# Optimization experiments

Measured on AMD Instinct MI355X. Metric: run time of the kernel, lower is better.

The kernel has to match this reference:

```python
import jax, jax.numpy as jnp
import numpy as np

N = 100000      # nodes
E = 1600000     # edges (avg degree 16)
IN = 128        # input_dim
H = 8           # heads
D = 8           # hidden_dim (== heads, required by the diversity-loss bmm)
HD = H * D      # per-layer width
OUT = 10        # output_dim
G = 64          # graphs in batch
NEG = 0.2       # GATConv leaky_relu slope
DIVW = 0.1      # diversity_weight


def setup_inputs() -> dict:
    key = jax.random.key(0)
    ks = jax.random.split(key, 20)
    w = lambda k, shape, fan: (jax.random.normal(k, shape, jnp.float32) / np.sqrt(fan)).astype(jnp.float32)
    inp = {}
    inp['x'] = jax.random.normal(ks[0], (N, IN), jnp.float32)
    inp['edge_index'] = jax.random.randint(ks[1], (2, E), 0, N, dtype=jnp.int32)
    inp['batch'] = jnp.sort(jax.random.randint(ks[2], (N,), 0, G, dtype=jnp.int32))
    # layer 0: GATConv(IN -> D, heads=H)
    inp['W0'] = w(ks[3], (IN, HD), IN)
    inp['att_src0'] = w(ks[4], (H, D), D)
    inp['att_dst0'] = w(ks[5], (H, D), D)
    inp['b0'] = jnp.zeros((HD,), jnp.float32)
    inp['gamma0'] = jnp.ones((HD,), jnp.float32)
    inp['beta0'] = jnp.zeros((HD,), jnp.float32)
    inp['P0'] = w(ks[6], (H, D), D)
    # layer 1: GATConv(HD -> D, heads=H)
    inp['W1'] = w(ks[7], (HD, HD), HD)
    inp['att_src1'] = w(ks[8], (H, D), D)
    inp['att_dst1'] = w(ks[9], (H, D), D)
    inp['b1'] = jnp.zeros((HD,), jnp.float32)
    inp['gamma1'] = jnp.ones((HD,), jnp.float32)
    inp['beta1'] = jnp.zeros((HD,), jnp.float32)
    inp['P1'] = w(ks[10], (H, D), D)
    inp['fc_W'] = w(ks[11], (HD, OUT), HD)
    inp['fc_b'] = jnp.zeros((OUT,), jnp.float32)
    return inp


def _gat(x, src, dst, W, a_src, a_dst, b):
    h = (x @ W).reshape(-1, H, D)                       # [N,H,D]
    al = jnp.sum(h * a_src, -1)                          # [N,H] src scores
    ar = jnp.sum(h * a_dst, -1)                          # [N,H] dst scores
    e = jax.nn.leaky_relu(al[src] + ar[dst], NEG)        # [E,H]
    m = jax.ops.segment_max(e, dst, num_segments=N)      # per-dst max (stable softmax)
    m = jnp.where(jnp.isfinite(m), m, 0.0)
    ex = jnp.exp(e - m[dst])
    den = jax.ops.segment_sum(ex, dst, num_segments=N)
    a = ex / (den[dst] + 1e-16)                          # PyG softmax eps
    out = jax.ops.segment_sum(a[:, :, None] * h[src], dst, num_segments=N)  # [N,H,D]
    return out.reshape(-1, HD) + b


def _bn(x, g, b):  # BatchNorm1d, training-mode batch stats, eps=1e-5
    mu = x.mean(0)
    var = x.var(0)
    return g * (x - mu) * jax.lax.rsqrt(var + 1e-5) + b


def _div_loss(x, P):
    xr = x.reshape(-1, H, D)
    pr = jnp.einsum('nij,jk->nik', xr, P)                # bmm with shared projector (needs D==H)
    nh = pr / jnp.maximum(jnp.linalg.norm(pr, axis=-1, keepdims=True), 1e-8)
    S = jnp.einsum('nid,njd->ij', nh, nh) / x.shape[0]   # mean-over-nodes cosine sims [H,H]
    iu = jnp.triu_indices(H, 1)
    return jnp.mean(S[iu] ** 2)


def reference(x, edge_index, batch, W0, att_src0, att_dst0, b0, gamma0, beta0, P0,
              W1, att_src1, att_dst1, b1, gamma1, beta1, P1, fc_W, fc_b):
    src, dst = edge_index[0], edge_index[1]
    dl = 0.0
    h = _gat(x, src, dst, W0, att_src0, att_dst0, b0)
    dl = dl + _div_loss(h, P0)
    h = jax.nn.elu(_bn(h, gamma0, beta0))
    h = _gat(h, src, dst, W1, att_src1, att_dst1, b1)
    dl = dl + _div_loss(h, P1)
    h = jax.nn.elu(_bn(h, gamma1, beta1))
    cnt = jax.ops.segment_sum(jnp.ones((N,), h.dtype), batch, num_segments=G)
    pooled = jax.ops.segment_sum(h, batch, num_segments=G) / jnp.maximum(cnt, 1.0)[:, None]
    logits = pooled @ fc_W + fc_b
    return logits, DIVW * dl
```

## Files before the change

### kernel.cpp

```cpp
#include <hip/hip_runtime.h>
#include <hip/hip_fp16.h>

#define NB 100000
#define NE 1600000
#define PSH 12500
#define BCAP 64
#define SCB 2048
#define GMB 1568
#define MIXB 3136

typedef int iv4 __attribute__((ext_vector_type(4)));

__device__ __forceinline__ float elu_f(float x) { return x > 0.f ? x : expm1f(x); }

__global__ __launch_bounds__(256) void k_fill_zero(float4* __restrict__ p, int n4) {
    int i = blockIdx.x * 256 + threadIdx.x, s = gridDim.x * 256;
    float4 z = make_float4(0.f, 0.f, 0.f, 0.f);
    for (; i < n4; i += s) p[i] = z;
}

__global__ __launch_bounds__(256) void k_scat_gemm(
    const iv4* __restrict__ src4, const iv4* __restrict__ dst4,
    int* __restrict__ cnt, int* __restrict__ buck, int ne4,
    const float* __restrict__ X, const float* __restrict__ W,
    const float* __restrict__ attS, const float* __restrict__ attD,
    __half* __restrict__ Hout, float* __restrict__ al, float* __restrict__ ar, int nrows)
{
    __shared__ float4 xs4[64][8];
    __shared__ float  ws_[32][64];
    int b = blockIdx.x, t = threadIdx.x;
    int isS, idx;
    if (b < MIXB) {
        int g = b >> 3;
        isS = g & 1;
        idx = (g >> 1) * 8 + (b & 7);
    } else {
        isS = 1;
        idx = GMB + (b - MIXB);
    }

    if (isS) {
        int part = idx & 7;
        unsigned lo = part * PSH;
        int pb = idx >> 3;
        int st = (SCB >> 3) * 256;
        int i  = pb * 256 + t;
        int i2 = i + st;
        int st2 = st * 2;
        for (; i2 < ne4; i += st2, i2 += st2) {
            iv4 dA = dst4[i];
            iv4 dB = dst4[i2];
            bool ax = (unsigned)(dA.x - lo) < PSH;
            bool ay = (unsigned)(dA.y - lo) < PSH;
            bool az = (unsigned)(dA.z - lo) < PSH;
            bool aw = (unsigned)(dA.w - lo) < PSH;
            bool bx = (unsigned)(dB.x - lo) < PSH;
            bool by = (unsigned)(dB.y - lo) < PSH;
            bool bz = (unsigned)(dB.z - lo) < PSH;
            bool bw = (unsigned)(dB.w - lo) < PSH;
            bool anyA = ax | ay | az | aw;
            bool anyB = bx | by | bz | bw;
            if (!(anyA | anyB)) continue;
            iv4 sA, sB;
            if (anyA) sA = src4[i];
            if (anyB) sB = src4[i2];
            int pax, pay, paz, paw, pbx, pby, pbz, pbw;
            if (ax) pax = atomicAdd(&cnt[dA.x], 1);
            if (ay) pay = atomicAdd(&cnt[dA.y], 1);
            if (az) paz = atomicAdd(&cnt[dA.z], 1);
            if (aw) paw = atomicAdd(&cnt[dA.w], 1);
            if (bx) pbx = atomicAdd(&cnt[dB.x], 1);
            if (by) pby = atomicAdd(&cnt[dB.y], 1);
            if (bz) pbz = atomicAdd(&cnt[dB.z], 1);
            if (bw) pbw = atomicAdd(&cnt[dB.w], 1);
            if (ax) buck[(dA.x << 6) + (pax & (BCAP - 1))] = sA.x;
            if (ay) buck[(dA.y << 6) + (pay & (BCAP - 1))] = sA.y;
            if (az) buck[(dA.z << 6) + (paz & (BCAP - 1))] = sA.z;
            if (aw) buck[(dA.w << 6) + (paw & (BCAP - 1))] = sA.w;
            if (bx) buck[(dB.x << 6) + (pbx & (BCAP - 1))] = sB.x;
            if (by) buck[(dB.y << 6) + (pby & (BCAP - 1))] = sB.y;
            if (bz) buck[(dB.z << 6) + (pbz & (BCAP - 1))] = sB.z;
            if (bw) buck[(dB.w << 6) + (pbw & (BCAP - 1))] = sB.w;
        }
        if (i < ne4) {
            iv4 d = dst4[i];
            bool cx = (unsigned)(d.x - lo) < PSH;
            bool cy = (unsigned)(d.y - lo) < PSH;
            bool cz = (unsigned)(d.z - lo) < PSH;
            bool cw = (unsigned)(d.w - lo) < PSH;
            if (cx | cy | cz | cw) {
                iv4 s = src4[i];
                if (cx) buck[(d.x << 6) + (atomicAdd(&cnt[d.x], 1) & (BCAP - 1))] = s.x;
                if (cy) buck[(d.y << 6) + (atomicAdd(&cnt[d.y], 1) & (BCAP - 1))] = s.y;
                if (cz) buck[(d.z << 6) + (atomicAdd(&cnt[d.z], 1) & (BCAP - 1))] = s.z;
                if (cw) buck[(d.w << 6) + (atomicAdd(&cnt[d.w], 1) & (BCAP - 1))] = s.w;
            }
        }
        return;
    }

    int rowBase = idx * 64;
    int r = t & 63, cg = t >> 6, c0 = cg * 16;
    float acc[16];
#pragma unroll
    for (int j = 0; j < 16; ++j) acc[j] = 0.f;
    int sw = r & 7;

    for (int kc = 0; kc < 4; ++kc) {
        if (kc) __syncthreads();
        for (int i = t; i < 512; i += 256)
            ((float4*)ws_)[i] = ((const float4*)W)[kc * 512 + i];
        for (int i = t; i < 512; i += 256) {
            int rr = i >> 3, c4 = i & 7;
            int gr = rowBase + rr;
            float4 v = make_float4(0.f, 0.f, 0.f, 0.f);
            if (gr < nrows) v = ((const float4*)X)[gr * 32 + kc * 8 + c4];
            xs4[rr][c4 ^ (rr & 7)] = v;
        }
        __syncthreads();
        for (int k4 = 0; k4 < 8; ++k4) {
            float4 xv = xs4[r][k4 ^ sw];
            float xk[4] = {xv.x, xv.y, xv.z, xv.w};
#pragma unroll
            for (int kk = 0; kk < 4; ++kk) {
                const float* wrow = &ws_[k4 * 4 + kk][c0];
                float4 wa = *(const float4*)(wrow + 0);
                float4 wb = *(const float4*)(wrow + 4);
                float4 wc = *(const float4*)(wrow + 8);
                float4 wd = *(const float4*)(wrow + 12);
                float x = xk[kk];
                acc[0]  += x * wa.x; acc[1]  += x * wa.y; acc[2]  += x * wa.z; acc[3]  += x * wa.w;
                acc[4]  += x * wb.x; acc[5]  += x * wb.y; acc[6]  += x * wb.z; acc[7]  += x * wb.w;
                acc[8]  += x * wc.x; acc[9]  += x * wc.y; acc[10] += x * wc.z; acc[11] += x * wc.w;
                acc[12] += x * wd.x; acc[13] += x * wd.y; acc[14] += x * wd.z; acc[15] += x * wd.w;
            }
        }
    }

    int gr = rowBase + r;
    if (gr < nrows) {
        __half2 hp[8];
#pragma unroll
        for (int j = 0; j < 8; ++j) hp[j] = __floats2half2_rn(acc[2 * j], acc[2 * j + 1]);
        uint4* op = (uint4*)(Hout + (size_t)gr * 64 + c0);
        op[0] = *(uint4*)&hp[0];
        op[1] = *(uint4*)&hp[4];
#pragma unroll
        for (int hh = 0; hh < 2; ++hh) {
            int h = cg * 2 + hh;
            float sa = 0.f, sd = 0.f;
#pragma unroll
            for (int d = 0; d < 8; ++d) {
                float hv = acc[hh * 8 + d];
                sa += hv * attS[h * 8 + d];
                sd += hv * attD[h * 8 + d];
            }
            al[gr * 8 + h] = sa;
            ar[gr * 8 + h] = sd;
        }
    }
}

__global__ __launch_bounds__(256) void k_gemm1(
    const float* __restrict__ X, const float* __restrict__ W,
    const float* __restrict__ attS, const float* __restrict__ attD,
    const float* __restrict__ bsum, const float* __restrict__ bsq,
    const float* __restrict__ gamma, const float* __restrict__ beta,
    __half* __restrict__ Hout, float* __restrict__ al, float* __restrict__ ar, int nrows)
{
    __shared__ float4 xs4[64][16];
    __shared__ float  ws_[64][64];
    __shared__ float  sc_[64], sh_[64];
    int t = threadIdx.x;
    int rowBase = blockIdx.x * 64;
    if (t < 64) {
        float invn = 1.f / (float)NB;
        float mu = bsum[t] * invn;
        float var = bsq[t] * invn - mu * mu;
        float s = gamma[t] * rsqrtf(var + 1e-5f);
        sc_[t] = s;
        sh_[t] = beta[t] - mu * s;
    }
    for (int i = t; i < 1024; i += 256)
        ((float4*)ws_)[i] = ((const float4*)W)[i];
    __syncthreads();

    for (int i = t; i < 1024; i += 256) {
        int rr = i >> 4, c4 = i & 15;
        int gr = rowBase + rr;
        float4 v = make_float4(0.f, 0.f, 0.f, 0.f);
        if (gr < nrows) v = ((const float4*)X)[gr * 16 + c4];
        int c = c4 * 4;
        v.x = elu_f(sc_[c + 0] * v.x + sh_[c + 0]);
        v.y = elu_f(sc_[c + 1] * v.y + sh_[c + 1]);
        v.z = elu_f(sc_[c + 2] * v.z + sh_[c + 2]);
        v.w = elu_f(sc_[c + 3] * v.w + sh_[c + 3]);
        xs4[rr][c4 ^ (rr & 15)] = v;
    }
    __syncthreads();

    int r = t & 63, cg = t >> 6, c0 = cg * 16;
    float acc[16];
#pragma unroll
    for (int j = 0; j < 16; ++j) acc[j] = 0.f;
    int sw = r & 15;
    for (int k4 = 0; k4 < 16; ++k4) {
        float4 xv = xs4[r][k4 ^ sw];
        float xk[4] = {xv.x, xv.y, xv.z, xv.w};
#pragma unroll
        for (int kk = 0; kk < 4; ++kk) {
            const float* wrow = &ws_[k4 * 4 + kk][c0];
            float4 wa = *(const float4*)(wrow + 0);
            float4 wb = *(const float4*)(wrow + 4);
            float4 wc = *(const float4*)(wrow + 8);
            float4 wd = *(const float4*)(wrow + 12);
            float x = xk[kk];
            acc[0]  += x * wa.x; acc[1]  += x * wa.y; acc[2]  += x * wa.z; acc[3]  += x * wa.w;
            acc[4]  += x * wb.x; acc[5]  += x * wb.y; acc[6]  += x * wb.z; acc[7]  += x * wb.w;
            acc[8]  += x * wc.x; acc[9]  += x * wc.y; acc[10] += x * wc.z; acc[11] += x * wc.w;
            acc[12] += x * wd.x; acc[13] += x * wd.y; acc[14] += x * wd.z; acc[15] += x * wd.w;
        }
    }
    int gr = rowBase + r;
    if (gr < nrows) {
        __half2 hp[8];
#pragma unroll
        for (int j = 0; j < 8; ++j) hp[j] = __floats2half2_rn(acc[2 * j], acc[2 * j + 1]);
        uint4* op = (uint4*)(Hout + (size_t)gr * 64 + c0);
        op[0] = *(uint4*)&hp[0];
        op[1] = *(uint4*)&hp[4];
#pragma unroll
        for (int hh = 0; hh < 2; ++hh) {
            int h = cg * 2 + hh;
            float sa = 0.f, sd = 0.f;
#pragma unroll
            for (int d = 0; d < 8; ++d) {
                float hv = acc[hh * 8 + d];
                sa += hv * attS[h * 8 + d];
                sd += hv * attD[h * 8 + d];
            }
            al[gr * 8 + h] = sa;
            ar[gr * 8 + h] = sd;
        }
    }
}

__global__ __launch_bounds__(256) void k_agg(const int* __restrict__ cnt, const int* __restrict__ buck,
    const float* __restrict__ al, const float* __restrict__ ar,
    const __half* __restrict__ Hf, const float* __restrict__ bias,
    float* __restrict__ agg, int n)
{
    int lane = threadIdx.x & 63;
    int w  = __builtin_amdgcn_readfirstlane((blockIdx.x * 256 + (int)threadIdx.x) >> 6);
    int nw = (gridDim.x * 256) >> 6;
    int h = lane >> 3;
    float bl = bias[lane];
    for (int d = w; d < n; d += nw) {
        int r0 = d << 6;
        int deg = __builtin_amdgcn_readfirstlane(cnt[d]);
        deg = deg < BCAP ? deg : BCAP;
        int r1 = r0 + deg;
        float arh = ar[d * 8 + h];
        float ac0 = 0.f, ac1 = 0.f, ac2 = 0.f, ac3 = 0.f, ac4 = 0.f, ac5 = 0.f, ac6 = 0.f, ac7 = 0.f;
        float de0 = 0.f, de1 = 0.f, de2 = 0.f, de3 = 0.f, de4 = 0.f, de5 = 0.f, de6 = 0.f, de7 = 0.f;
        int p = r0;
        for (; p + 8 <= r1; p += 8) {
            int s0 = __builtin_amdgcn_readfirstlane(buck[p]);
            int s1 = __builtin_amdgcn_readfirstlane(buck[p + 1]);
            int s2 = __builtin_amdgcn_readfirstlane(buck[p + 2]);
            int s3 = __builtin_amdgcn_readfirstlane(buck[p + 3]);
            int s4 = __builtin_amdgcn_readfirstlane(buck[p + 4]);
            int s5 = __builtin_amdgcn_readfirstlane(buck[p + 5]);
            int s6 = __builtin_amdgcn_readfirstlane(buck[p + 6]);
            int s7 = __builtin_amdgcn_readfirstlane(buck[p + 7]);
            float t0 = al[s0 * 8 + h] + arh;
            float t1 = al[s1 * 8 + h] + arh;
            float t2 = al[s2 * 8 + h] + arh;
            float t3 = al[s3 * 8 + h] + arh;
            float t4 = al[s4 * 8 + h] + arh;
            float t5 = al[s5 * 8 + h] + arh;
            float t6 = al[s6 * 8 + h] + arh;
            float t7 = al[s7 * 8 + h] + arh;
            float h0 = __half2float(Hf[((size_t)s0 << 6) + lane]);
            float h1 = __half2float(Hf[((size_t)s1 << 6) + lane]);
            float h2 = __half2float(Hf[((size_t)s2 << 6) + lane]);
            float h3 = __half2float(Hf[((size_t)s3 << 6) + lane]);
            float h4 = __half2float(Hf[((size_t)s4 << 6) + lane]);
            float h5 = __half2float(Hf[((size_t)s5 << 6) + lane]);
            float h6 = __half2float(Hf[((size_t)s6 << 6) + lane]);
            float h7 = __half2float(Hf[((size_t)s7 << 6) + lane]);
            t0 = t0 > 0.f ? t0 : 0.2f * t0;  t1 = t1 > 0.f ? t1 : 0.2f * t1;
            t2 = t2 > 0.f ? t2 : 0.2f * t2;  t3 = t3 > 0.f ? t3 : 0.2f * t3;
            t4 = t4 > 0.f ? t4 : 0.2f * t4;  t5 = t5 > 0.f ? t5 : 0.2f * t5;
            t6 = t6 > 0.f ? t6 : 0.2f * t6;  t7 = t7 > 0.f ? t7 : 0.2f * t7;
            float e0 = __expf(t0), e1 = __expf(t1), e2 = __expf(t2), e3 = __expf(t3);
            float e4 = __expf(t4), e5 = __expf(t5), e6 = __expf(t6), e7 = __expf(t7);
            de0 += e0; ac0 = fmaf(e0, h0, ac0);
            de1 += e1; ac1 = fmaf(e1, h1, ac1);
            de2 += e2; ac2 = fmaf(e2, h2, ac2);
            de3 += e3; ac3 = fmaf(e3, h3, ac3);
            de4 += e4; ac4 = fmaf(e4, h4, ac4);
            de5 += e5; ac5 = fmaf(e5, h5, ac5);
            de6 += e6; ac6 = fmaf(e6, h6, ac6);
            de7 += e7; ac7 = fmaf(e7, h7, ac7);
        }
        for (; p + 4 <= r1; p += 4) {
            int s0 = __builtin_amdgcn_readfirstlane(buck[p]);
            int s1 = __builtin_amdgcn_readfirstlane(buck[p + 1]);
            int s2 = __builtin_amdgcn_readfirstlane(buck[p + 2]);
            int s3 = __builtin_amdgcn_readfirstlane(buck[p + 3]);
            float t0 = al[s0 * 8 + h] + arh;
            float t1 = al[s1 * 8 + h] + arh;
            float t2 = al[s2 * 8 + h] + arh;
            float t3 = al[s3 * 8 + h] + arh;
            float h0 = __half2float(Hf[((size_t)s0 << 6) + lane]);
            float h1 = __half2float(Hf[((size_t)s1 << 6) + lane]);
            float h2 = __half2float(Hf[((size_t)s2 << 6) + lane]);
            float h3 = __half2float(Hf[((size_t)s3 << 6) + lane]);
            t0 = t0 > 0.f ? t0 : 0.2f * t0;  t1 = t1 > 0.f ? t1 : 0.2f * t1;
            t2 = t2 > 0.f ? t2 : 0.2f * t2;  t3 = t3 > 0.f ? t3 : 0.2f * t3;
            float e0 = __expf(t0), e1 = __expf(t1), e2 = __expf(t2), e3 = __expf(t3);
            de0 += e0; ac0 = fmaf(e0, h0, ac0);
            de1 += e1; ac1 = fmaf(e1, h1, ac1);
            de2 += e2; ac2 = fmaf(e2, h2, ac2);
            de3 += e3; ac3 = fmaf(e3, h3, ac3);
        }
        for (; p < r1; ++p) {
            int s0 = __builtin_amdgcn_readfirstlane(buck[p]);
            float t0 = al[s0 * 8 + h] + arh;
            float h0 = __half2float(Hf[((size_t)s0 << 6) + lane]);
            t0 = t0 > 0.f ? t0 : 0.2f * t0;
            float e0 = __expf(t0);
            de0 += e0; ac0 = fmaf(e0, h0, ac0);
        }
        float den = ((de0 + de1) + (de2 + de3)) + ((de4 + de5) + (de6 + de7));
        float num = ((ac0 + ac1) + (ac2 + ac3)) + ((ac4 + ac5) + (ac6 + ac7));
        float inv = 1.f / (den + 1e-16f);
        agg[(size_t)d * 64 + lane] = fmaf(num, inv, bl);
    }
}

__global__ __launch_bounds__(256) void k_post(const float* __restrict__ agg, const float* __restrict__ P,
    float* __restrict__ Sord, float* __restrict__ bsum, float* __restrict__ bsq, int n)
{
    __shared__ float Ps[64];
    __shared__ float red[4][184];
    int t = threadIdx.x;
    if (t < 64) Ps[t] = P[t];
    __syncthreads();
    int lane = t & 63, wid = t >> 6;
    int h = lane & 7, grp = lane >> 3;
    int w  = (blockIdx.x * 256 + t) >> 6;
    int nw = (gridDim.x * 256) >> 6;
    float sacc[7], bs[8], bq[8];
#pragma unroll
    for (int i = 0; i < 7; ++i) sacc[i] = 0.f;
#pragma unroll
    for (int i = 0; i < 8; ++i) { bs[i] = 0.f; bq[i] = 0.f; }

    for (int base = w * 8; base < n; base += nw * 8) {
        int node = base + grp;
        float xv[8];
        if (node < n) {
            const float4* rp = (const float4*)(agg + (size_t)node * 64 + h * 8);
            float4 a = rp[0], b = rp[1];
            xv[0]=a.x; xv[1]=a.y; xv[2]=a.z; xv[3]=a.w; xv[4]=b.x; xv[5]=b.y; xv[6]=b.z; xv[7]=b.w;
        } else {
#pragma unroll
            for (int k = 0; k < 8; ++k) xv[k] = 0.f;
        }
#pragma unroll
        for (int k = 0; k < 8; ++k) { bs[k] += xv[k]; bq[k] += xv[k] * xv[k]; }
        float pr[8];
#pragma unroll
        for (int k = 0; k < 8; ++k) pr[k] = 0.f;
#pragma unroll
        for (int j = 0; j < 8; ++j) {
            float x = xv[j];
#pragma unroll
            for (int k = 0; k < 8; ++k) pr[k] += x * Ps[j * 8 + k];
        }
        float nrm2 = 0.f;
#pragma unroll
        for (int k = 0; k < 8; ++k) nrm2 += pr[k] * pr[k];
        float inv = 1.f / fmaxf(sqrtf(nrm2), 1e-8f);
#pragma unroll
        for (int k = 0; k < 8; ++k) pr[k] *= inv;
#pragma unroll
        for (int d = 1; d < 8; ++d) {
            float dot = 0.f;
#pragma unroll
            for (int k = 0; k < 8; ++k) dot += pr[k] * __shfl_xor(pr[k], d, 64);
            sacc[d - 1] += dot;
        }
    }
#pragma unroll
    for (int d = 0; d < 7; ++d) {
        sacc[d] += __shfl_xor(sacc[d], 8, 64);
        sacc[d] += __shfl_xor(sacc[d], 16, 64);
        sacc[d] += __shfl_xor(sacc[d], 32, 64);
    }
#pragma unroll
    for (int k = 0; k < 8; ++k) {
        bs[k] += __shfl_xor(bs[k], 8, 64); bs[k] += __shfl_xor(bs[k], 16, 64); bs[k] += __shfl_xor(bs[k], 32, 64);
        bq[k] += __shfl_xor(bq[k], 8, 64); bq[k] += __shfl_xor(bq[k], 16, 64); bq[k] += __shfl_xor(bq[k], 32, 64);
    }
    if (lane < 8) {
#pragma unroll
        for (int d = 0; d < 7; ++d) red[wid][h * 23 + d] = sacc[d];
#pragma unroll
        for (int k = 0; k < 8; ++k) { red[wid][h * 23 + 7 + k] = bs[k]; red[wid][h * 23 + 15 + k] = bq[k]; }
    }
    __syncthreads();
    if (t < 184) {
        float v = red[0][t] + red[1][t] + red[2][t] + red[3][t];
        int hh = t / 23, r = t % 23;
        if (r < 7)       atomicAdd(&Sord[hh * 8 + (hh ^ (r + 1))], v);
        else if (r < 15) atomicAdd(&bsum[hh * 8 + (r - 7)], v);
        else             atomicAdd(&bsq [hh * 8 + (r - 15)], v);
    }
}

__global__ __launch_bounds__(256) void k_pool(const float* __restrict__ agg, const int* __restrict__ batch,
    const float* __restrict__ bsum, const float* __restrict__ bsq,
    const float* __restrict__ gamma, const float* __restrict__ beta,
    float* __restrict__ psum, float* __restrict__ cnt, int n)
{
    int lane = threadIdx.x & 63;
    int w  = (blockIdx.x * 256 + threadIdx.x) >> 6;
    int nw = (gridDim.x * 256) >> 6;
    int chunk = (n + nw - 1) / nw;
    int n0 = w * chunk;
    if (n0 >= n) return;
    int n1 = min(n, n0 + chunk);
    float invn = 1.f / (float)n;
    float mu = bsum[lane] * invn;
    float var = bsq[lane] * invn - mu * mu;
    float sc = gamma[lane] * rsqrtf(var + 1e-5f);
    float sh = beta[lane] - mu * sc;
    float acc = 0.f;
    int curg = batch[n0], run = 0;
    for (int i = n0; i < n1; ++i) {
        int g = batch[i];
        if (g != curg) {
            atomicAdd(psum + curg * 64 + lane, acc);
            if (lane == 0) atomicAdd(cnt + curg, (float)run);
            acc = 0.f; run = 0; curg = g;
        }
        float v = agg[(size_t)i * 64 + lane];
        v = sc * v + sh;
        v = v > 0.f ? v : expm1f(v);
        acc += v; run += 1;
    }
    atomicAdd(psum + curg * 64 + lane, acc);
    if (lane == 0) atomicAdd(cnt + curg, (float)run);
}

__global__ __launch_bounds__(640) void k_final(const float* __restrict__ psum, const float* __restrict__ cnt,
    const float* __restrict__ fcW, const float* __restrict__ fcb,
    const float* __restrict__ S0, const float* __restrict__ S1,
    float* __restrict__ out, int n)
{
    __shared__ float pl[64][65];
    int t = threadIdx.x;
    for (int i = t; i < 4096; i += 640) {
        int g = i >> 6, c = i & 63;
        pl[g][c] = psum[i] / fmaxf(cnt[g], 1.f);
    }
    __syncthreads();
    {
        int g = t / 10, o = t % 10;
        float s = fcb[o];
#pragma unroll 8
        for (int c = 0; c < 64; ++c) s += pl[g][c] * fcW[c * 10 + o];
        out[g * 10 + o] = s;
    }
    if (t == 0) {
        float invn = 1.f / (float)n;
        float dl = 0.f;
        for (int i = 0; i < 8; ++i)
            for (int j = i + 1; j < 8; ++j) {
                float v0 = S0[i * 8 + j] * invn; dl += v0 * v0;
                float v1 = S1[i * 8 + j] * invn; dl += v1 * v1;
            }
        out[640] = 0.1f * (dl / 28.f);
    }
}

extern "C" void kernel_launch(void* const* d_in, const int* in_sizes, int n_in,
                              void* d_out, int out_size, void* d_ws, size_t ws_size,
                              hipStream_t stream)
{
    const float* x   = (const float*)d_in[0];
    const int*   ei  = (const int*)d_in[1];
    const int*   bat = (const int*)d_in[2];
    const float* W0  = (const float*)d_in[3];
    const float* as0 = (const float*)d_in[4];
    const float* ad0 = (const float*)d_in[5];
    const float* b0  = (const float*)d_in[6];
    const float* g0  = (const float*)d_in[7];
    const float* be0 = (const float*)d_in[8];
    const float* P0  = (const float*)d_in[9];
    const float* W1  = (const float*)d_in[10];
    const float* as1 = (const float*)d_in[11];
    const float* ad1 = (const float*)d_in[12];
    const float* b1  = (const float*)d_in[13];
    const float* g1  = (const float*)d_in[14];
    const float* be1 = (const float*)d_in[15];
    const float* P1  = (const float*)d_in[16];
    const float* fcW = (const float*)d_in[17];
    const float* fcb = (const float*)d_in[18];
    const int* src = ei;
    const int* dst = ei + NE;

    float* ws    = (float*)d_ws;
    __half* Hbuf = (__half*)ws;
    float* agg   = ws + 6400000;
    float* al    = ws + 12800000;
    float* ar    = ws + 13600000;
    float* stats = ws + 14400000;
    float* psum  = ws + 14401024;
    int*   cnt   = (int*)(ws + 14405120);
    int*   buck  = cnt + NB;

    float* Sord0 = stats + 0;
    float* Sord1 = stats + 64;
    float* sum0  = stats + 128;
    float* sq0   = stats + 192;
    float* sum1  = stats + 256;
    float* sq1   = stats + 320;
    float* gcnt  = stats + 640;

    k_fill_zero<<<103, 256, 0, stream>>>((float4*)stats, 26280);

    k_scat_gemm<<<SCB + GMB, 256, 0, stream>>>((const iv4*)src, (const iv4*)dst, cnt, buck, NE / 4,
                                               x, W0, as0, ad0, Hbuf, al, ar, NB);

    k_agg<<<25000, 256, 0, stream>>>(cnt, buck, al, ar, Hbuf, b0, agg, NB);
    k_post<<<512, 256, 0, stream>>>(agg, P0, Sord0, sum0, sq0, NB);

    k_gemm1<<<1563, 256, 0, stream>>>(agg, W1, as1, ad1, sum0, sq0, g0, be0, Hbuf, al, ar, NB);
    k_agg<<<25000, 256, 0, stream>>>(cnt, buck, al, ar, Hbuf, b1, agg, NB);
    k_post<<<512, 256, 0, stream>>>(agg, P1, Sord1, sum1, sq1, NB);

    k_pool<<<512, 256, 0, stream>>>(agg, bat, sum1, sq1, g1, be1, psum, gcnt, NB);
    k_final<<<1, 640, 0, stream>>>(psum, gcnt, fcW, fcb, Sord0, Sord1, (float*)d_out, NB);
}
```

Measured before the change: 327.8 us.

## Fuse BatchNorm statistics into aggregation and merge diversity-loss and pooling into one tail

Each aggregation kernel now computes per-block column sums and sums of squares for BatchNorm and writes them to a partial buffer. A small reduction kernel then finishes those sums, so the per-layer post kernel no longer has to re-read the aggregated features before the next GEMM. Both diversity-loss passes and the final pooling move into a single role-split tail kernel that runs after the second layer. This needs a second aggregation buffer and a partial-sum buffer. The sum of squares is taken from a per-wave running sum, which is only correct when each wave handles exactly one node.

```diff
diff --git a/kernel.cpp b/kernel.cpp
--- a/kernel.cpp
+++ b/kernel.cpp
@@ -248,13 +248,16 @@
 __global__ __launch_bounds__(256) void k_agg(const int* __restrict__ cnt, const int* __restrict__ buck,
     const float* __restrict__ al, const float* __restrict__ ar,
     const __half* __restrict__ Hf, const float* __restrict__ bias,
-    float* __restrict__ agg, int n)
+    float* __restrict__ agg, float* __restrict__ partial, int n)
 {
-    int lane = threadIdx.x & 63;
-    int w  = __builtin_amdgcn_readfirstlane((blockIdx.x * 256 + (int)threadIdx.x) >> 6);
+    __shared__ float redp[4][128];
+    int t = threadIdx.x;
+    int lane = t & 63, wid = t >> 6;
+    int w  = __builtin_amdgcn_readfirstlane((blockIdx.x * 256 + t) >> 6);
     int nw = (gridDim.x * 256) >> 6;
     int h = lane >> 3;
     float bl = bias[lane];
+    float val = 0.f;
     for (int d = w; d < n; d += nw) {
         int r0 = d << 6;
         int deg = __builtin_amdgcn_readfirstlane(cnt[d]);
@@ -336,27 +339,99 @@
         float den = ((de0 + de1) + (de2 + de3)) + ((de4 + de5) + (de6 + de7));
         float num = ((ac0 + ac1) + (ac2 + ac3)) + ((ac4 + ac5) + (ac6 + ac7));
         float inv = 1.f / (den + 1e-16f);
-        agg[(size_t)d * 64 + lane] = fmaf(num, inv, bl);
-    }
-}
-
-__global__ __launch_bounds__(256) void k_post(const float* __restrict__ agg, const float* __restrict__ P,
-    float* __restrict__ Sord, float* __restrict__ bsum, float* __restrict__ bsq, int n)
+        float v = fmaf(num, inv, bl);
+        agg[(size_t)d * 64 + lane] = v;
+        val += v;
+        redp[wid][lane] = 0.f;
+    }
+    {
+        float bsv = val;
+        float bqv = 0.f;
+        bqv = val * val;
+        redp[wid][lane]      = bsv;
+        redp[wid][64 + lane] = bqv;
+    }
+    __syncthreads();
+    if (t < 128) {
+        float s = redp[0][t] + redp[1][t] + redp[2][t] + redp[3][t];
+        partial[(size_t)blockIdx.x * 128 + t] = s;
+    }
+}
+
+__global__ __launch_bounds__(256) void k_bnred(const float* __restrict__ partial,
+                                               float* __restrict__ bsum, float* __restrict__ bsq) {
+    __shared__ float sh[256];
+    int t = threadIdx.x, c = t & 127, half = t >> 7;
+    int rbase = blockIdx.x * 125;
+    float acc = 0.f;
+    for (int r = rbase + half; r < rbase + 125; r += 2)
+        acc += partial[(size_t)r * 128 + c];
+    sh[t] = acc;
+    __syncthreads();
+    if (t < 128) {
+        float v = sh[t] + sh[t + 128];
+        if (t < 64) atomicAdd(&bsum[t], v);
+        else        atomicAdd(&bsq[t - 64], v);
+    }
+}
+
+__global__ __launch_bounds__(256) void k_tail(
+    const float* __restrict__ agg0, const float* __restrict__ agg1,
+    const float* __restrict__ P0, const float* __restrict__ P1,
+    float* __restrict__ Sord0, float* __restrict__ Sord1,
+    const int* __restrict__ batch,
+    const float* __restrict__ bsum, const float* __restrict__ bsq,
+    const float* __restrict__ gamma, const float* __restrict__ beta,
+    float* __restrict__ psum, float* __restrict__ cnt, int n)
 {
+    int role = blockIdx.x % 3;
+    int idx  = blockIdx.x / 3;
+    int t = threadIdx.x;
+    int lane = t & 63, wid = t >> 6;
+    const int nw = 2048;
+
+    if (role == 2) {
+        int w = (idx * 256 + t) >> 6;
+        int chunk = (n + nw - 1) / nw;
+        int n0 = w * chunk;
+        if (n0 >= n) return;
+        int n1 = min(n, n0 + chunk);
+        float invn = 1.f / (float)n;
+        float mu = bsum[lane] * invn;
+        float var = bsq[lane] * invn - mu * mu;
+        float sc = gamma[lane] * rsqrtf(var + 1e-5f);
+        float sh = beta[lane] - mu * sc;
+        float acc = 0.f;
+        int curg = batch[n0], run = 0;
+        for (int i = n0; i < n1; ++i) {
+            int g = batch[i];
+            if (g != curg) {
+                atomicAdd(psum + curg * 64 + lane, acc);
+                if (lane == 0) atomicAdd(cnt + curg, (float)run);
+                acc = 0.f; run = 0; curg = g;
+            }
+            float v = agg1[(size_t)i * 64 + lane];
+            v = sc * v + sh;
+            v = v > 0.f ? v : expm1f(v);
+            acc += v; run += 1;
+        }
+        atomicAdd(psum + curg * 64 + lane, acc);
+        if (lane == 0) atomicAdd(cnt + curg, (float)run);
+        return;
+    }
+
+    const float* agg = role ? agg1 : agg0;
+    const float* P   = role ? P1 : P0;
+    float* Sord      = role ? Sord1 : Sord0;
     __shared__ float Ps[64];
-    __shared__ float red[4][184];
-    int t = threadIdx.x;
+    __shared__ float red[4][56];
     if (t < 64) Ps[t] = P[t];
     __syncthreads();
-    int lane = t & 63, wid = t >> 6;
     int h = lane & 7, grp = lane >> 3;
-    int w  = (blockIdx.x * 256 + t) >> 6;
-    int nw = (gridDim.x * 256) >> 6;
-    float sacc[7], bs[8], bq[8];
+    int w = (idx * 256 + t) >> 6;
+    float sacc[7];
 #pragma unroll
     for (int i = 0; i < 7; ++i) sacc[i] = 0.f;
-#pragma unroll
-    for (int i = 0; i < 8; ++i) { bs[i] = 0.f; bq[i] = 0.f; }
 
     for (int base = w * 8; base < n; base += nw * 8) {
         int node = base + grp;
@@ -369,8 +444,6 @@
 #pragma unroll
             for (int k = 0; k < 8; ++k) xv[k] = 0.f;
         }
-#pragma unroll
-        for (int k = 0; k < 8; ++k) { bs[k] += xv[k]; bq[k] += xv[k] * xv[k]; }
         float pr[8];
 #pragma unroll
         for (int k = 0; k < 8; ++k) pr[k] = 0.f;
@@ -400,60 +473,16 @@
         sacc[d] += __shfl_xor(sacc[d], 16, 64);
         sacc[d] += __shfl_xor(sacc[d], 32, 64);
     }
-#pragma unroll
-    for (int k = 0; k < 8; ++k) {
-        bs[k] += __shfl_xor(bs[k], 8, 64); bs[k] += __shfl_xor(bs[k], 16, 64); bs[k] += __shfl_xor(bs[k], 32, 64);
-        bq[k] += __shfl_xor(bq[k], 8, 64); bq[k] += __shfl_xor(bq[k], 16, 64); bq[k] += __shfl_xor(bq[k], 32, 64);
-    }
     if (lane < 8) {
 #pragma unroll
-        for (int d = 0; d < 7; ++d) red[wid][h * 23 + d] = sacc[d];
-#pragma unroll
-        for (int k = 0; k < 8; ++k) { red[wid][h * 23 + 7 + k] = bs[k]; red[wid][h * 23 + 15 + k] = bq[k]; }
-    }
-    __syncthreads();
-    if (t < 184) {
+        for (int d = 0; d < 7; ++d) red[wid][h * 7 + d] = sacc[d];
+    }
+    __syncthreads();
+    if (t < 56) {
         float v = red[0][t] + red[1][t] + red[2][t] + red[3][t];
-        int hh = t / 23, r = t % 23;
-        if (r < 7)       atomicAdd(&Sord[hh * 8 + (hh ^ (r + 1))], v);
-        else if (r < 15) atomicAdd(&bsum[hh * 8 + (r - 7)], v);
-        else             atomicAdd(&bsq [hh * 8 + (r - 15)], v);
-    }
-}
-
-__global__ __launch_bounds__(256) void k_pool(const float* __restrict__ agg, const int* __restrict__ batch,
-    const float* __restrict__ bsum, const float* __restrict__ bsq,
-    const float* __restrict__ gamma, const float* __restrict__ beta,
-    float* __restrict__ psum, float* __restrict__ cnt, int n)
-{
-    int lane = threadIdx.x & 63;
-    int w  = (blockIdx.x * 256 + threadIdx.x) >> 6;
-    int nw = (gridDim.x * 256) >> 6;
-    int chunk = (n + nw - 1) / nw;
-    int n0 = w * chunk;
-    if (n0 >= n) return;
-    int n1 = min(n, n0 + chunk);
-    float invn = 1.f / (float)n;
-    float mu = bsum[lane] * invn;
-    float var = bsq[lane] * invn - mu * mu;
-    float sc = gamma[lane] * rsqrtf(var + 1e-5f);
-    float sh = beta[lane] - mu * sc;
-    float acc = 0.f;
-    int curg = batch[n0], run = 0;
-    for (int i = n0; i < n1; ++i) {
-        int g = batch[i];
-        if (g != curg) {
-            atomicAdd(psum + curg * 64 + lane, acc);
-            if (lane == 0) atomicAdd(cnt + curg, (float)run);
-            acc = 0.f; run = 0; curg = g;
-        }
-        float v = agg[(size_t)i * 64 + lane];
-        v = sc * v + sh;
-        v = v > 0.f ? v : expm1f(v);
-        acc += v; run += 1;
-    }
-    atomicAdd(psum + curg * 64 + lane, acc);
-    if (lane == 0) atomicAdd(cnt + curg, (float)run);
+        int hh = t / 7, r = t % 7;
+        atomicAdd(&Sord[hh * 8 + (hh ^ (r + 1))], v);
+    }
 }
 
 __global__ __launch_bounds__(640) void k_final(const float* __restrict__ psum, const float* __restrict__ cnt,
@@ -515,13 +544,15 @@
 
     float* ws    = (float*)d_ws;
     __half* Hbuf = (__half*)ws;
-    float* agg   = ws + 6400000;
-    float* al    = ws + 12800000;
-    float* ar    = ws + 13600000;
-    float* stats = ws + 14400000;
-    float* psum  = ws + 14401024;
-    int*   cnt   = (int*)(ws + 14405120);
+    float* agg0  = ws + 3200000;
+    float* agg1  = ws + 9600000;
+    float* al    = ws + 16000000;
+    float* ar    = ws + 16800000;
+    float* stats = ws + 17600000;
+    float* psum  = ws + 17601024;
+    int*   cnt   = (int*)(ws + 17605120);
     int*   buck  = cnt + NB;
+    float* partial = (float*)(buck + (size_t)NB * 64);
 
     float* Sord0 = stats + 0;
     float* Sord1 = stats + 64;
@@ -536,13 +567,14 @@
     k_scat_gemm<<<SCB + GMB, 256, 0, stream>>>((const iv4*)src, (const iv4*)dst, cnt, buck, NE / 4,
                                                x, W0, as0, ad0, Hbuf, al, ar, NB);
 
-    k_agg<<<25000, 256, 0, stream>>>(cnt, buck, al, ar, Hbuf, b0, agg, NB);
-    k_post<<<512, 256, 0, stream>>>(agg, P0, Sord0, sum0, sq0, NB);
-
-    k_gemm1<<<1563, 256, 0, stream>>>(agg, W1, as1, ad1, sum0, sq0, g0, be0, Hbuf, al, ar, NB);
-    k_agg<<<25000, 256, 0, stream>>>(cnt, buck, al, ar, Hbuf, b1, agg, NB);
-    k_post<<<512, 256, 0, stream>>>(agg, P1, Sord1, sum1, sq1, NB);
-
-    k_pool<<<512, 256, 0, stream>>>(agg, bat, sum1, sq1, g1, be1, psum, gcnt, NB);
+    k_agg<<<25000, 256, 0, stream>>>(cnt, buck, al, ar, Hbuf, b0, agg0, partial, NB);
+    k_bnred<<<200, 256, 0, stream>>>(partial, sum0, sq0);
+
+    k_gemm1<<<1563, 256, 0, stream>>>(agg0, W1, as1, ad1, sum0, sq0, g0, be0, Hbuf, al, ar, NB);
+    k_agg<<<25000, 256, 0, stream>>>(cnt, buck, al, ar, Hbuf, b1, agg1, partial, NB);
+    k_bnred<<<200, 256, 0, stream>>>(partial, sum1, sq1);
+
+    k_tail<<<1536, 256, 0, stream>>>(agg0, agg1, P0, P1, Sord0, Sord1, bat,
+                                     sum1, sq1, g1, be1, psum, gcnt, NB);
     k_final<<<1, 640, 0, stream>>>(psum, gcnt, fcW, fcb, Sord0, Sord1, (float*)d_out, NB);
 }
```

Measured after the change: 338.1 us. 3.1% more time.
